# Optimization experiments

Measured on AMD Instinct MI355X. Metric: run time of the kernel, lower is better.

## Reference

```python
import jax, jax.numpy as jnp
import numpy as np

T, A, B_IMG, Z, READ_N, WRITE_N, ENC, DEC, BATCH = 16, 64, 64, 128, 8, 8, 512, 512, 512
EPS = 1e-8


def setup_inputs() -> dict:
    key = jax.random.key(0)
    ks = jax.random.split(key, 16)
    s = 0.05
    n = lambda k, shape: jax.random.normal(k, shape, jnp.float32) * s
    return {
        "x": jax.random.uniform(ks[0], (BATCH, B_IMG * A), jnp.float32),
        "eps": jax.random.normal(ks[1], (T, BATCH, Z), jnp.float32),
        "enc_Wih": n(ks[2], (4 * ENC, 2 * READ_N * READ_N + DEC)),
        "enc_Whh": n(ks[3], (4 * ENC, ENC)),
        "enc_b": jnp.zeros((4 * ENC,), jnp.float32),
        "mu_W": n(ks[4], (Z, ENC)),
        "mu_b": jnp.zeros((Z,), jnp.float32),
        "sig_W": n(ks[5], (Z, ENC)),
        "sig_b": jnp.zeros((Z,), jnp.float32),
        "dec_Wih": n(ks[6], (4 * DEC, Z)),
        "dec_Whh": n(ks[7], (4 * DEC, DEC)),
        "dec_b": jnp.zeros((4 * DEC,), jnp.float32),
        "write_W": n(ks[8], (WRITE_N * WRITE_N, DEC)),
        "write_b": jnp.zeros((WRITE_N * WRITE_N,), jnp.float32),
        "attn_W": n(ks[9], (5, DEC)),
        "attn_b": jnp.zeros((5,), jnp.float32),
    }


def _lstm(x, h, c, Wih, Whh, b):
    g = x @ Wih.T + h @ Whh.T + b  # [bs, 4H]
    i, f, gg, o = jnp.split(g, 4, axis=1)
    c2 = jax.nn.sigmoid(f) * c + jax.nn.sigmoid(i) * jnp.tanh(gg)
    return jax.nn.sigmoid(o) * jnp.tanh(c2), c2


def _filterbank(gx, gy, sigma2, delta, N):
    # gx, gy, sigma2, delta: [bs, 1]
    grid = jnp.arange(N, dtype=jnp.float32)[None, :]  # [1, N]
    mu_x = gx + (grid - 0.5 * N - 0.5) * delta  # [bs, N]
    mu_y = gy + (grid - 0.5 * N - 0.5) * delta
    a = jnp.arange(A, dtype=jnp.float32)
    b = jnp.arange(B_IMG, dtype=jnp.float32)
    s2 = sigma2[:, :, None]  # [bs,1,1]
    Fx = jnp.exp(-((a[None, None, :] - mu_x[:, :, None]) ** 2) / (2 * s2))  # [bs,N,A]
    Fx = Fx / (Fx.sum(2, keepdims=True) + EPS)
    Fy = jnp.exp(-((b[None, None, :] - mu_y[:, :, None]) ** 2) / (2 * s2))  # [bs,N,B]
    Fy = Fy / (Fy.sum(2, keepdims=True) + EPS)
    return Fx, Fy


def _attn_window(h_dec, N, attn_W, attn_b):
    p = h_dec @ attn_W.T + attn_b  # [bs,5]
    gx_, gy_, log_s2, log_d, log_g = jnp.split(p, 5, axis=1)
    gx = (A + 1) * 0.5 * (gx_ + 1)
    gy = (B_IMG + 1) * 0.5 * (gy_ + 1)
    delta = (max(A, B_IMG) - 1) * jnp.exp(log_d) / (N - 1)
    Fx, Fy = _filterbank(gx, gy, jnp.exp(log_s2), delta, N)
    return Fx, Fy, jnp.exp(log_g)  # gamma: [bs,1]


def reference(x, eps, enc_Wih, enc_Whh, enc_b, mu_W, mu_b, sig_W, sig_b,
              dec_Wih, dec_Whh, dec_b, write_W, write_b, attn_W, attn_b):
    bs = x.shape[0]
    img = x.reshape(bs, B_IMG, A)

    def step(carry, e):
        h_enc, c_enc, h_dec, c_dec, canvas = carry
        x_hat = x - jax.nn.sigmoid(canvas)
        # --- read with attention ---
        Fx, Fy, gamma = _attn_window(h_dec, READ_N, attn_W, attn_b)
        def glimpse(im):  # Fy @ im @ Fx^T -> [bs, N, N]
            g = jnp.einsum('bnh,bhw,bmw->bnm', Fy, im, Fx)
            return g.reshape(bs, READ_N * READ_N) * gamma
        r = jnp.concatenate([glimpse(img), glimpse(x_hat.reshape(bs, B_IMG, A))], axis=1)
        # --- encoder LSTM ---
        h_enc, c_enc = _lstm(jnp.concatenate([r, h_dec], 1), h_enc, c_enc, enc_Wih, enc_Whh, enc_b)
        # --- latent sample ---
        mu = h_enc @ mu_W.T + mu_b
        log_sigma = h_enc @ sig_W.T + sig_b
        z = mu + e * jnp.exp(log_sigma)
        # --- decoder LSTM ---
        h_dec, c_dec = _lstm(z, h_dec, c_dec, dec_Wih, dec_Whh, dec_b)
        # --- write with attention ---
        w = (h_dec @ write_W.T + write_b).reshape(bs, WRITE_N, WRITE_N)
        Fx2, Fy2, gamma2 = _attn_window(h_dec, WRITE_N, attn_W, attn_b)
        wr = jnp.einsum('bnh,bnm,bma->bha', Fy2, w, Fx2).reshape(bs, B_IMG * A) / gamma2
        canvas = canvas + wr
        return (h_enc, c_enc, h_dec, c_dec, canvas), canvas

    z32 = jnp.zeros((bs, ENC), jnp.float32)
    init = (z32, z32, jnp.zeros((bs, DEC), jnp.float32), jnp.zeros((bs, DEC), jnp.float32),
            jnp.zeros((bs, B_IMG * A), jnp.float32))
    _, cs = jax.lax.scan(step, init, eps)
    return cs  # [T, bs, B*A]
```

## Files before the change

kernel.cpp:

```cpp
#include <hip/hip_runtime.h>

#define LDF 68
#define EPSF 1e-8f
#define MFMA(A,B,C) __builtin_amdgcn_mfma_f32_16x16x32_bf16((A),(B),(C),0,0,0)

typedef __attribute__((ext_vector_type(8))) short bf16x8;
typedef __attribute__((ext_vector_type(4))) float f32x4;

__device__ __forceinline__ float sigf(float x){ return 1.0f/(1.0f + __expf(-x)); }

__device__ __forceinline__ unsigned short f2bf(float f){
  unsigned u = __float_as_uint(f);
  u += 0x7FFFu + ((u >> 16) & 1u);
  return (unsigned short)(u >> 16);
}
__device__ __forceinline__ float bf2f(unsigned short s){
  return __uint_as_float((unsigned)s << 16);
}

__device__ __forceinline__ size_t pk(int b, int col, int KB){
  return ((((size_t)((b>>4)*KB + (col>>5)))*64) + (size_t)((b&15) + (((col>>3)&3)<<4)))*8 + (col&7);
}

__device__ __forceinline__ void gload_lds16(const void* g, void* l){
  __builtin_amdgcn_global_load_lds(
      (const __attribute__((address_space(1))) void*)g,
      (__attribute__((address_space(3))) void*)l, 16, 0, 0);
}

__global__ void pack_w_mfma(const float* __restrict__ Wih, const float* __restrict__ Whh,
                            int K_ih, int K_tot,
                            unsigned short* __restrict__ dhi, unsigned short* __restrict__ dlo,
                            int total8){
  int idx = blockIdx.x*256 + threadIdx.x;
  if (idx >= total8) return;
  int lane = idx & 63;
  int rest = idx >> 6;
  int KB = K_tot >> 5;
  int kb = rest % KB;
  int fm = rest / KB;
  int rr = fm*16 + (lane & 15);
  int orow = (rr & 3)*512 + (rr >> 2);
  int k0 = kb*32 + (lane >> 4)*8;
  union { unsigned short s[8]; uint4 u; } vh, vl;
  #pragma unroll
  for (int i = 0; i < 8; i++){
    int k = k0 + i;
    float f = (k < K_ih) ? Wih[(size_t)orow*K_ih + k]
                         : Whh[(size_t)orow*512 + (k - K_ih)];
    unsigned short hi = f2bf(f);
    vh.s[i] = hi;
    vl.s[i] = f2bf(f - bf2f(hi));
  }
  *(uint4*)(dhi + (size_t)idx*8) = vh.u;
  *(uint4*)(dlo + (size_t)idx*8) = vl.u;
}

__global__ void init_misc(const float* __restrict__ enc_b, const float* __restrict__ dec_b,
                          const float* __restrict__ writeW,
                          const float* __restrict__ muW, const float* __restrict__ sigW,
                          float* __restrict__ bE, float* __restrict__ bD,
                          float* __restrict__ WwT,
                          unsigned short* __restrict__ Wzh, unsigned short* __restrict__ Wzl){
  int idx = blockIdx.x*256 + threadIdx.x;
  if (idx < 2048){
    bE[idx] = enc_b[(idx & 3)*512 + (idx >> 2)];
    return;
  }
  idx -= 2048;
  if (idx < 2048){
    bD[idx] = dec_b[(idx & 3)*512 + (idx >> 2)];
    return;
  }
  idx -= 2048;
  if (idx < 32768){
    int k = idx >> 6, n = idx & 63;
    WwT[idx] = writeW[n*512 + k];
    return;
  }
  idx -= 32768;
  if (idx < 16384){
    int lane = idx & 63, rest = idx >> 6;
    int kb = rest & 15, fmf = rest >> 4;
    int row = fmf*16 + (lane & 15);
    const float* src = (row < 128) ? (muW + (size_t)row*512) : (sigW + (size_t)(row-128)*512);
    int k0 = kb*32 + (lane >> 4)*8;
    union { unsigned short s[8]; uint4 u; } vh, vl;
    #pragma unroll
    for (int i = 0; i < 8; i++){
      float f = src[k0 + i];
      unsigned short hi = f2bf(f);
      vh.s[i] = hi;
      vl.s[i] = f2bf(f - bf2f(hi));
    }
    *(uint4*)(Wzh + (size_t)idx*8) = vh.u;
    *(uint4*)(Wzl + (size_t)idx*8) = vl.u;
  }
}

__global__ void zero_f(float* p, int n){
  int idx = blockIdx.x*256 + threadIdx.x;
  if (idx < n) p[idx] = 0.f;
}

template<int KB>
__global__ __launch_bounds__(512) void mfma_gemm_lstm(
    const bf16x8* __restrict__ Wh, const bf16x8* __restrict__ Wl,
    const unsigned short* __restrict__ act, int actPlane,
    const float4* __restrict__ bias4, const float* __restrict__ c_in,
    float* __restrict__ h_f32, float* __restrict__ c_out,
    unsigned short* __restrict__ out0, int KB0, int off0, int plane0,
    unsigned short* __restrict__ out1, int KB1, int off1, int plane1)
{
  __shared__ __align__(16) unsigned char lds[3][8192];
  const int tid = threadIdx.x, lane = tid & 63, w = tid >> 6;
  const int mt = blockIdx.x & 31, nt = blockIdx.x >> 5;
  const int fm = w & 3, fn0 = (w >> 2) << 1;

  const bf16x8* whp = Wh + ((size_t)(mt*4+fm)*KB)*64 + lane;
  const bf16x8* wlp = Wl + ((size_t)(mt*4+fm)*KB)*64 + lane;
  const char* ast = (const char*)act + (size_t)(w & 1)*((size_t)actPlane*2)
                  + ((size_t)(nt*4 + (w >> 1))*KB)*1024 + (size_t)lane*16;

  const int j0 = (mt*4+fm)*4 + (lane >> 4);
  float4 bb = bias4[j0];
  f32x4 acc0 = {bb.x, bb.y, bb.z, bb.w};
  f32x4 acc1 = acc0;

  gload_lds16(ast, (char*)&lds[0][w*1024]);
  bf16x8 whA = whp[0], wlA = wlp[0];
  __builtin_amdgcn_sched_barrier(0);
  asm volatile("" ::: "memory");
  gload_lds16(ast + 1024, (char*)&lds[1][w*1024]);
  bf16x8 whB = whp[64], wlB = wlp[64];
  __builtin_amdgcn_sched_barrier(0);
  asm volatile("" ::: "memory");

  const size_t rdoff = (size_t)fn0*2048 + (size_t)lane*16;

  #pragma unroll
  for (int kb = 0; kb < KB; kb++){
    if (kb + 1 < KB) asm volatile("s_waitcnt vmcnt(3)" ::: "memory");
    else             asm volatile("s_waitcnt vmcnt(0)" ::: "memory");
    __builtin_amdgcn_s_barrier();
    asm volatile("" ::: "memory");
    __builtin_amdgcn_sched_barrier(0);
    bf16x8 whC = whA, wlC = wlA;
    if (kb + 2 < KB){
      gload_lds16(ast + (size_t)(kb+2)*1024, (char*)&lds[(kb+2)%3][w*1024]);
      whC = whp[(kb+2)*64]; wlC = wlp[(kb+2)*64];
    }
    const unsigned char* rb = &lds[kb%3][0] + rdoff;
    bf16x8 a0h = *(const bf16x8*)(rb);
    bf16x8 a0l = *(const bf16x8*)(rb + 1024);
    bf16x8 a1h = *(const bf16x8*)(rb + 2048);
    bf16x8 a1l = *(const bf16x8*)(rb + 3072);
    acc0 = MFMA(whA, a0h, acc0);
    acc1 = MFMA(whA, a1h, acc1);
    acc0 = MFMA(wlA, a0h, acc0);
    acc1 = MFMA(wlA, a1h, acc1);
    acc0 = MFMA(whA, a0l, acc0);
    acc1 = MFMA(whA, a1l, acc1);
    whA = whB; wlA = wlB; whB = whC; wlB = wlC;
  }

  const int bb0 = nt*64 + fn0*16 + (lane & 15);
  #pragma unroll
  for (int n = 0; n < 2; n++){
    f32x4 g = n ? acc1 : acc0;
    int b = bb0 + n*16;
    float ig = sigf(g[0]);
    float fg = sigf(g[1]);
    float gg = tanhf(g[2]);
    float og = sigf(g[3]);
    float c2 = fg * c_in[(size_t)b*512 + j0] + ig * gg;
    float h  = og * tanhf(c2);
    c_out[(size_t)b*512 + j0] = c2;
    if (h_f32) h_f32[(size_t)b*512 + j0] = h;
    unsigned short hh = f2bf(h);
    unsigned short hl = f2bf(h - bf2f(hh));
    size_t o0 = pk(b, off0 + j0, KB0);
    out0[o0] = hh; out0[o0 + plane0] = hl;
    if (out1){
      size_t o1 = pk(b, off1 + j0, KB1);
      out1[o1] = hh; out1[o1 + plane1] = hl;
    }
  }
}

__global__ __launch_bounds__(512) void zgemm8(
    const unsigned short* __restrict__ Wzh, const unsigned short* __restrict__ Wzl,
    const unsigned short* __restrict__ az, int planeZ,
    const float* __restrict__ mu_b, const float* __restrict__ sig_b,
    const float* __restrict__ eps_t,
    unsigned short* __restrict__ actD, int planeD)
{
  __shared__ float zred[8*64*8];
  const int tid = threadIdx.x, lane = tid & 63, w = tid >> 6;
  const int fmb = blockIdx.x & 7, cg = blockIdx.x >> 3;
  const char* azh = (const char*)az + (size_t)cg*16384 + (size_t)lane*16;
  const char* azl = (const char*)(az + planeZ) + (size_t)cg*16384 + (size_t)lane*16;
  const int kb0 = w*2;

  bf16x8 a0h = *(const bf16x8*)(azh + (size_t)kb0*1024);
  bf16x8 a0l = *(const bf16x8*)(azl + (size_t)kb0*1024);
  bf16x8 a1h = *(const bf16x8*)(azh + (size_t)(kb0+1)*1024);
  bf16x8 a1l = *(const bf16x8*)(azl + (size_t)(kb0+1)*1024);

  const bf16x8* wmh = (const bf16x8*)Wzh + (size_t)(fmb    *16)*64 + lane;
  const bf16x8* wml = (const bf16x8*)Wzl + (size_t)(fmb    *16)*64 + lane;
  const bf16x8* wsh = (const bf16x8*)Wzh + (size_t)((fmb+8)*16)*64 + lane;
  const bf16x8* wsl = (const bf16x8*)Wzl + (size_t)((fmb+8)*16)*64 + lane;
  bf16x8 m0h = wmh[kb0*64],     m0l = wml[kb0*64];
  bf16x8 s0h = wsh[kb0*64],     s0l = wsl[kb0*64];
  bf16x8 m1h = wmh[(kb0+1)*64], m1l = wml[(kb0+1)*64];
  bf16x8 s1h = wsh[(kb0+1)*64], s1l = wsl[(kb0+1)*64];

  f32x4 am = {0.f,0.f,0.f,0.f}, as = {0.f,0.f,0.f,0.f};
  am = MFMA(m0h,a0h,am); am = MFMA(m0l,a0h,am); am = MFMA(m0h,a0l,am);
  as = MFMA(s0h,a0h,as); as = MFMA(s0l,a0h,as); as = MFMA(s0h,a0l,as);
  am = MFMA(m1h,a1h,am); am = MFMA(m1l,a1h,am); am = MFMA(m1h,a1l,am);
  as = MFMA(s1h,a1h,as); as = MFMA(s1l,a1h,as); as = MFMA(s1h,a1l,as);

  *(f32x4*)&zred[(size_t)(w*64+lane)*8]     = am;
  *(f32x4*)&zred[(size_t)(w*64+lane)*8 + 4] = as;
  __syncthreads();

  if (w == 0){
    const int r0 = fmb*16 + (lane >> 4)*4;
    float4 bm = *(const float4*)&mu_b[r0];
    float4 bs = *(const float4*)&sig_b[r0];
    f32x4 AM = {bm.x,bm.y,bm.z,bm.w};
    f32x4 AS = {bs.x,bs.y,bs.z,bs.w};
    #pragma unroll
    for (int v = 0; v < 8; v++){
      AM += *(f32x4*)&zred[(size_t)(v*64+lane)*8];
      AS += *(f32x4*)&zred[(size_t)(v*64+lane)*8 + 4];
    }
    const int b = cg*16 + (lane & 15);
    float4 ev = *(const float4*)&eps_t[(size_t)b*128 + r0];
    float e[4] = {ev.x, ev.y, ev.z, ev.w};
    union { unsigned short s[4]; uint2 u; } zh, zl;
    #pragma unroll
    for (int i = 0; i < 4; i++){
      float z = AM[i] + e[i]*__expf(AS[i]);
      unsigned short hi = f2bf(z);
      zh.s[i] = hi;
      zl.s[i] = f2bf(z - bf2f(hi));
    }
    size_t o = pk(b, r0, 20);
    *(uint2*)(actD + o) = zh.u;
    *(uint2*)(actD + planeD + o) = zl.u;
  }
}

__device__ void attn_window(const float* __restrict__ h,
                            const float* __restrict__ attn_W,
                            const float* __restrict__ attn_b,
                            float* Fx, float* Fy, float* pl)
{
  int tid = threadIdx.x;
  int lane = tid & 63, wid = tid >> 6;
  for (int q = wid; q < 5; q += 4){
    float s = 0.f;
    for (int k = lane; k < 512; k += 64) s += h[k]*attn_W[q*512 + k];
    for (int m = 32; m; m >>= 1) s += __shfl_xor(s, m);
    if (lane == 0) pl[q] = s + attn_b[q];
  }
  __syncthreads();
  float gx    = 32.5f*(pl[0] + 1.f);
  float gy    = 32.5f*(pl[1] + 1.f);
  float s2    = __expf(pl[2]);
  float delta = 9.f*__expf(pl[3]);
  float inv2  = 1.f/(2.f*s2);
  int n = tid >> 5, a = tid & 31;
  float mux = gx + ((float)n - 4.5f)*delta;
  float muy = gy + ((float)n - 4.5f)*delta;
  float dx0 = (float)a      - mux, dx1 = (float)(a+32) - mux;
  float dy0 = (float)a      - muy, dy1 = (float)(a+32) - muy;
  float e0 = __expf(-dx0*dx0*inv2), e1 = __expf(-dx1*dx1*inv2);
  float f0 = __expf(-dy0*dy0*inv2), f1 = __expf(-dy1*dy1*inv2);
  float sx = e0 + e1, sy = f0 + f1;
  for (int m = 16; m; m >>= 1){ sx += __shfl_xor(sx, m); sy += __shfl_xor(sy, m); }
  float rx = 1.f/(sx + EPSF), ry = 1.f/(sy + EPSF);
  Fx[n*LDF + a]      = e0*rx;  Fx[n*LDF + a + 32] = e1*rx;
  Fy[n*LDF + a]      = f0*ry;  Fy[n*LDF + a + 32] = f1*ry;
  __syncthreads();
}

__global__ __launch_bounds__(256) void wg_kernel(
    const float* __restrict__ h_dec,
    const float* __restrict__ WwT, const float* __restrict__ write_b,
    const float* __restrict__ attn_W, const float* __restrict__ attn_b,
    const float* __restrict__ canvas_prev, float* __restrict__ canvas_out,
    const float* __restrict__ x,
    unsigned short* __restrict__ rout, int planeE)
{
  __shared__ float hs[512];
  __shared__ float Fx[8*LDF], Fy[8*LDF], pl[8];
  __shared__ float cs[64*LDF];
  __shared__ float img_s[64*LDF];
  __shared__ float P[2][8*LDF];
  __shared__ float ps[4][64], w_s[64];
  __shared__ float tmp[64*8];
  const int b = blockIdx.x, tid = threadIdx.x;

  for (int i = tid; i < 128; i += 256)
    ((float4*)hs)[i] = ((const float4*)(h_dec + (size_t)b*512))[i];
  if (rout){
    const float4* x4 = (const float4*)(x + (size_t)b*4096);
    for (int i = tid; i < 1024; i += 256){
      int row = i >> 4, cb = (i & 15)*4;
      *(float4*)&img_s[row*LDF + cb] = x4[i];
    }
  }
  __syncthreads();
  attn_window(hs, attn_W, attn_b, Fx, Fy, pl);
  float gamma = __expf(pl[4]);

  if (canvas_out){
    {
      int j = tid & 63, part = tid >> 6;
      float s = 0.f;
      int kb = part*128;
      for (int k = 0; k < 128; k++) s += hs[kb + k] * WwT[(kb + k)*64 + j];
      ps[part][j] = s;
    }
    __syncthreads();
    if (tid < 64)
      w_s[tid] = write_b[tid] + ps[0][tid] + ps[1][tid] + ps[2][tid] + ps[3][tid];
    __syncthreads();
    float inv_g = __expf(-pl[4]);
    #pragma unroll
    for (int e = 0; e < 2; e++){
      int gi = e*256 + tid;
      int m = gi & 7, hh = gi >> 3;
      float s = 0.f;
      #pragma unroll
      for (int nn = 0; nn < 8; nn++) s += Fy[nn*LDF + hh] * w_s[nn*8 + m];
      tmp[hh*8 + m] = s;
    }
    __syncthreads();
    for (int e = 0; e < 16; e++){
      int idx = e*256 + tid;
      int hh = idx >> 6, a = idx & 63;
      float s = 0.f;
      #pragma unroll
      for (int m = 0; m < 8; m++) s += tmp[hh*8 + m] * Fx[m*LDF + a];
      float prev = canvas_prev ? canvas_prev[(size_t)b*4096 + idx] : 0.f;
      float cv = prev + s*inv_g;
      canvas_out[(size_t)b*4096 + idx] = cv;
      cs[hh*LDF + a] = cv;
    }
  } else {
    for (int e = 0; e < 16; e++){
      int idx = e*256 + tid;
      cs[(idx >> 6)*LDF + (idx & 63)] = 0.f;
    }
  }
  if (!rout) return;
  __syncthreads();
  for (int e = 0; e < 16; e++){
    int idx = e*256 + tid;
    int hh = idx >> 6, a = idx & 63;
    cs[hh*LDF + a] = sigf(cs[hh*LDF + a]);
  }
  __syncthreads();
  #pragma unroll
  for (int e = 0; e < 4; e++){
    int gi = e*256 + tid;
    int d = gi >> 9, rem = gi & 511;
    int m = rem & 7, hh = rem >> 3;
    const float* S = d ? cs : img_s;
    float s = 0.f;
    #pragma unroll
    for (int w4 = 0; w4 < 64; w4 += 4){
      float4 iv = *(const float4*)&S[hh*LDF + w4];
      float4 fv = *(const float4*)&Fx[m*LDF + w4];
      s += iv.x*fv.x + iv.y*fv.y + iv.z*fv.z + iv.w*fv.w;
    }
    P[d][m*LDF + hh] = s;
  }
  __syncthreads();
  if (tid < 128){
    int d = tid >> 6, l = tid & 63;
    int n = l >> 3, m = l & 7;
    float s = 0.f;
    #pragma unroll
    for (int h4 = 0; h4 < 64; h4 += 4){
      float4 fv = *(const float4*)&Fy[n*LDF + h4];
      float4 pv = *(const float4*)&P[d][m*LDF + h4];
      s += fv.x*pv.x + fv.y*pv.y + fv.z*pv.z + fv.w*pv.w;
    }
    tmp[d*64 + l] = s;
  }
  __syncthreads();
  if (tid < 64){
    float g1 = tmp[tid]*gamma;
    float g2 = (tmp[tid] - tmp[64 + tid])*gamma;
    unsigned short h1 = f2bf(g1), l1 = f2bf(g1 - bf2f(h1));
    unsigned short h2 = f2bf(g2), l2 = f2bf(g2 - bf2f(h2));
    size_t o1 = pk(b, tid, 36);
    size_t o2 = pk(b, 64 + tid, 36);
    rout[o1] = h1; rout[o1 + planeE] = l1;
    rout[o2] = h2; rout[o2 + planeE] = l2;
  }
}

extern "C" void kernel_launch(void* const* d_in, const int* in_sizes, int n_in,
                              void* d_out, int out_size, void* d_ws, size_t ws_size,
                              hipStream_t stream)
{
  (void)in_sizes; (void)n_in; (void)out_size; (void)ws_size;
  const float* x       = (const float*)d_in[0];
  const float* eps     = (const float*)d_in[1];
  const float* encWih  = (const float*)d_in[2];
  const float* encWhh  = (const float*)d_in[3];
  const float* enc_b   = (const float*)d_in[4];
  const float* muW     = (const float*)d_in[5];
  const float* mu_b    = (const float*)d_in[6];
  const float* sigW    = (const float*)d_in[7];
  const float* sig_b   = (const float*)d_in[8];
  const float* decWih  = (const float*)d_in[9];
  const float* decWhh  = (const float*)d_in[10];
  const float* dec_b   = (const float*)d_in[11];
  const float* writeW  = (const float*)d_in[12];
  const float* write_b = (const float*)d_in[13];
  const float* attnW   = (const float*)d_in[14];
  const float* attn_b  = (const float*)d_in[15];
  float* out = (float*)d_out;

  char* p = (char*)d_ws;
  auto alloc = [&](size_t bytes){ char* r = p; p += (bytes + 255) & ~(size_t)255; return r; };

  const int KE = 1152, KD = 640;
  const int PE = 512*KE, PD = 512*KD, PZ = 512*512;
  const int T8E = 128*36*64, T8D = 128*20*64;

  unsigned short* WpEh = (unsigned short*)alloc((size_t)T8E*16);
  unsigned short* WpEl = (unsigned short*)alloc((size_t)T8E*16);
  unsigned short* WpDh = (unsigned short*)alloc((size_t)T8D*16);
  unsigned short* WpDl = (unsigned short*)alloc((size_t)T8D*16);
  unsigned short* Wzh  = (unsigned short*)alloc(16384*16);
  unsigned short* Wzl  = (unsigned short*)alloc(16384*16);
  float* bE  = (float*)alloc(2048*4);
  float* bD  = (float*)alloc(2048*4);
  float* WwT = (float*)alloc(512*64*4);
  char* z0 = p;
  unsigned short* actE0 = (unsigned short*)alloc((size_t)2*PE*2);
  unsigned short* actD0 = (unsigned short*)alloc((size_t)2*PD*2);
  float* hDf = (float*)alloc(512*512*4);
  float* cE0 = (float*)alloc(512*512*4);
  float* cD0 = (float*)alloc(512*512*4);
  size_t zbytes = (size_t)(p - z0);
  unsigned short* actE1 = (unsigned short*)alloc((size_t)2*PE*2);
  unsigned short* actD1 = (unsigned short*)alloc((size_t)2*PD*2);
  unsigned short* AZ    = (unsigned short*)alloc((size_t)2*PZ*2);
  float* cE1 = (float*)alloc(512*512*4);
  float* cD1 = (float*)alloc(512*512*4);

  unsigned short* actE[2] = { actE0, actE1 };
  unsigned short* actD[2] = { actD0, actD1 };
  float* cEf[2] = { cE0, cE1 };
  float* cDf[2] = { cD0, cD1 };

  int tot;
  tot = T8E;   pack_w_mfma<<<(tot+255)/256,256,0,stream>>>(encWih, encWhh, 640, KE, WpEh, WpEl, tot);
  tot = T8D;   pack_w_mfma<<<(tot+255)/256,256,0,stream>>>(decWih, decWhh, 128, KD, WpDh, WpDl, tot);
  tot = 2048+2048+32768+16384;
  init_misc<<<(tot+255)/256,256,0,stream>>>(enc_b, dec_b, writeW, muW, sigW,
                                            bE, bD, WwT, Wzh, Wzl);
  tot = (int)(zbytes/4); zero_f<<<(tot+255)/256,256,0,stream>>>((float*)z0, tot);

  wg_kernel<<<512,256,0,stream>>>(hDf, WwT, write_b, attnW, attn_b,
                                  nullptr, nullptr, x, actE[0], PE);

  for (int t = 0; t < 16; t++){
    int cur = t & 1, nxt = cur ^ 1;

    mfma_gemm_lstm<36><<<256,512,0,stream>>>(
        (const bf16x8*)WpEh, (const bf16x8*)WpEl, actE[cur], PE,
        (const float4*)bE, cEf[cur], nullptr, cEf[nxt],
        AZ, 16, 0, PZ,
        actE[nxt], 36, 640, PE);

    zgemm8<<<256,512,0,stream>>>(
        Wzh, Wzl, AZ, PZ, mu_b, sig_b,
        eps + (size_t)t*65536, actD[cur], PD);

    mfma_gemm_lstm<20><<<256,512,0,stream>>>(
        (const bf16x8*)WpDh, (const bf16x8*)WpDl, actD[cur], PD,
        (const float4*)bD, cDf[cur], hDf, cDf[nxt],
        actE[nxt], 36, 128, PE,
        actD[nxt], 20, 128, PD);

    wg_kernel<<<512,256,0,stream>>>(hDf, WwT, write_b, attnW, attn_b,
                                    t ? (out + (size_t)(t-1)*2097152) : nullptr,
                                    out + (size_t)t*2097152, x,
                                    (t < 15) ? actE[nxt] : nullptr, PE);
  }
}
```

Before: 881.6 us.

## Process two k-blocks per pipeline stage in LSTM GEMM and use fast tanh

Restructures the LSTM MFMA GEMM pipeline so each stage loads and consumes two k-blocks, halving the barrier and wait overhead per iteration, and doubles the LDS stage buffers accordingly. Adds a launch bound hint for occupancy and replaces tanhf with an exp-based fast approximation in the gate epilogue. The change risks register pressure and slightly different numerics near tanh saturation, and it assumes KB is even.

Measured after the change: 889.7 us. No clear change (+0.9%).

```diff
diff --git a/kernel.cpp b/kernel.cpp
--- a/kernel.cpp
+++ b/kernel.cpp
@@ -8,6 +8,7 @@
 typedef __attribute__((ext_vector_type(4))) float f32x4;
 
 __device__ __forceinline__ float sigf(float x){ return 1.0f/(1.0f + __expf(-x)); }
+__device__ __forceinline__ float tanhfast(float x){ return 1.f - 2.f/(1.f + __expf(2.f*x)); }
 
 __device__ __forceinline__ unsigned short f2bf(float f){
   unsigned u = __float_as_uint(f);
@@ -104,7 +105,7 @@
 }
 
 template<int KB>
-__global__ __launch_bounds__(512) void mfma_gemm_lstm(
+__global__ __launch_bounds__(512, 4) void mfma_gemm_lstm(
     const bf16x8* __restrict__ Wh, const bf16x8* __restrict__ Wl,
     const unsigned short* __restrict__ act, int actPlane,
     const float4* __restrict__ bias4, const float* __restrict__ c_in,
@@ -112,7 +113,8 @@
     unsigned short* __restrict__ out0, int KB0, int off0, int plane0,
     unsigned short* __restrict__ out1, int KB1, int off1, int plane1)
 {
-  __shared__ __align__(16) unsigned char lds[3][8192];
+  constexpr int NI = KB/2;
+  __shared__ __align__(16) unsigned char lds[3][16384];
   const int tid = threadIdx.x, lane = tid & 63, w = tid >> 6;
   const int mt = blockIdx.x & 31, nt = blockIdx.x >> 5;
   const int fm = w & 3, fn0 = (w >> 2) << 1;
@@ -127,41 +129,60 @@
   f32x4 acc0 = {bb.x, bb.y, bb.z, bb.w};
   f32x4 acc1 = acc0;
 
-  gload_lds16(ast, (char*)&lds[0][w*1024]);
-  bf16x8 whA = whp[0], wlA = wlp[0];
+  bf16x8 wh[2][2], wl[2][2];
+
+  wh[0][0] = whp[0];  wh[0][1] = whp[64];
+  wl[0][0] = wlp[0];  wl[0][1] = wlp[64];
   __builtin_amdgcn_sched_barrier(0);
-  asm volatile("" ::: "memory");
-  gload_lds16(ast + 1024, (char*)&lds[1][w*1024]);
-  bf16x8 whB = whp[64], wlB = wlp[64];
+  {
+    char* d0 = (char*)&lds[0][w*2048];
+    gload_lds16(ast,        d0);
+    gload_lds16(ast + 1024, d0 + 1024);
+  }
   __builtin_amdgcn_sched_barrier(0);
-  asm volatile("" ::: "memory");
-
-  const size_t rdoff = (size_t)fn0*2048 + (size_t)lane*16;
+  {
+    char* d1 = (char*)&lds[1][w*2048];
+    gload_lds16(ast + 2048, d1);
+    gload_lds16(ast + 3072, d1 + 1024);
+  }
+  __builtin_amdgcn_sched_barrier(0);
+
+  const size_t rdbase = (size_t)fn0*4096 + (size_t)lane*16;
 
   #pragma unroll
-  for (int kb = 0; kb < KB; kb++){
-    if (kb + 1 < KB) asm volatile("s_waitcnt vmcnt(3)" ::: "memory");
-    else             asm volatile("s_waitcnt vmcnt(0)" ::: "memory");
+  for (int i = 0; i < NI; i++){
+    if (i + 1 < NI) asm volatile("s_waitcnt vmcnt(2)" ::: "memory");
+    else            asm volatile("s_waitcnt vmcnt(0)" ::: "memory");
     __builtin_amdgcn_s_barrier();
-    asm volatile("" ::: "memory");
     __builtin_amdgcn_sched_barrier(0);
-    bf16x8 whC = whA, wlC = wlA;
-    if (kb + 2 < KB){
-      gload_lds16(ast + (size_t)(kb+2)*1024, (char*)&lds[(kb+2)%3][w*1024]);
-      whC = whp[(kb+2)*64]; wlC = wlp[(kb+2)*64];
-    }
-    const unsigned char* rb = &lds[kb%3][0] + rdoff;
-    bf16x8 a0h = *(const bf16x8*)(rb);
-    bf16x8 a0l = *(const bf16x8*)(rb + 1024);
-    bf16x8 a1h = *(const bf16x8*)(rb + 2048);
-    bf16x8 a1l = *(const bf16x8*)(rb + 3072);
-    acc0 = MFMA(whA, a0h, acc0);
-    acc1 = MFMA(whA, a1h, acc1);
-    acc0 = MFMA(wlA, a0h, acc0);
-    acc1 = MFMA(wlA, a1h, acc1);
-    acc0 = MFMA(whA, a0l, acc0);
-    acc1 = MFMA(whA, a1l, acc1);
-    whA = whB; wlA = wlB; whB = whC; wlB = wlC;
+    if (i + 1 < NI){
+      wh[(i+1)&1][0] = whp[(2*i+2)*64];
+      wh[(i+1)&1][1] = whp[(2*i+3)*64];
+      wl[(i+1)&1][0] = wlp[(2*i+2)*64];
+      wl[(i+1)&1][1] = wlp[(2*i+3)*64];
+    }
+    __builtin_amdgcn_sched_barrier(0);
+    if (i + 2 < NI){
+      char* dst = (char*)&lds[(i+2)%3][w*2048];
+      gload_lds16(ast + (size_t)(2*i+4)*1024, dst);
+      gload_lds16(ast + (size_t)(2*i+5)*1024, dst + 1024);
+    }
+    __builtin_amdgcn_sched_barrier(0);
+    const unsigned char* rb = &lds[i%3][0] + rdbase;
+    #pragma unroll
+    for (int kbi = 0; kbi < 2; kbi++){
+      bf16x8 a0h = *(const bf16x8*)(rb +        kbi*1024);
+      bf16x8 a0l = *(const bf16x8*)(rb + 2048 + kbi*1024);
+      bf16x8 a1h = *(const bf16x8*)(rb + 4096 + kbi*1024);
+      bf16x8 a1l = *(const bf16x8*)(rb + 6144 + kbi*1024);
+      bf16x8 WH = wh[i&1][kbi], WL = wl[i&1][kbi];
+      acc0 = MFMA(WH, a0h, acc0);
+      acc1 = MFMA(WH, a1h, acc1);
+      acc0 = MFMA(WL, a0h, acc0);
+      acc1 = MFMA(WL, a1h, acc1);
+      acc0 = MFMA(WH, a0l, acc0);
+      acc1 = MFMA(WH, a1l, acc1);
+    }
   }
 
   const int bb0 = nt*64 + fn0*16 + (lane & 15);
@@ -171,10 +192,10 @@
     int b = bb0 + n*16;
     float ig = sigf(g[0]);
     float fg = sigf(g[1]);
-    float gg = tanhf(g[2]);
+    float gg = tanhfast(g[2]);
     float og = sigf(g[3]);
     float c2 = fg * c_in[(size_t)b*512 + j0] + ig * gg;
-    float h  = og * tanhf(c2);
+    float h  = og * tanhfast(c2);
     c_out[(size_t)b*512 + j0] = c2;
     if (h_f32) h_f32[(size_t)b*512 + j0] = h;
     unsigned short hh = f2bf(h);
```

## Fuse decoder LSTM GEMM with write/glimpse kernel via per-batch-tile grid barrier

Applied to the files above, without the earlier changes.

Merges the decoder LSTM GEMM and the attention write/read kernel into one launch. Blocks that share a batch tile sync through a global atomic counter, then each block handles the write and glimpse stage for two batch rows, reading h_dec with cache-bypassing loads. This removes one kernel launch and its gap per timestep and lets the write work start per tile instead of after the whole GEMM. It also swaps tanhf for an exp-based fast tanh. The spin barrier assumes all 32 blocks of a tile are co-resident, so the code risks deadlock and a little precision loss.

Measured after the change: 1.008 ms. 14.3% more time.

```diff
diff --git a/kernel.cpp b/kernel.cpp
--- a/kernel.cpp
+++ b/kernel.cpp
@@ -8,6 +8,7 @@
 typedef __attribute__((ext_vector_type(4))) float f32x4;
 
 __device__ __forceinline__ float sigf(float x){ return 1.0f/(1.0f + __expf(-x)); }
+__device__ __forceinline__ float tanhfast(float x){ return 1.f - 2.f/(1.f + __expf(2.f*x)); }
 
 __device__ __forceinline__ unsigned short f2bf(float f){
   unsigned u = __float_as_uint(f);
@@ -26,6 +27,15 @@
   __builtin_amdgcn_global_load_lds(
       (const __attribute__((address_space(1))) void*)g,
       (__attribute__((address_space(3))) void*)l, 16, 0, 0);
+}
+
+__device__ __forceinline__ uint4 ld_x4_sc(const void* p){
+  uint4 r;
+  asm volatile("global_load_dwordx4 %0, %1, off sc0 sc1" : "=v"(r) : "v"(p));
+  return r;
+}
+__device__ __forceinline__ void st_dword_sc(void* p, float v){
+  asm volatile("global_store_dword %0, %1, off sc0 sc1" :: "v"(p), "v"(v) : "memory");
 }
 
 __global__ void pack_w_mfma(const float* __restrict__ Wih, const float* __restrict__ Whh,
@@ -104,15 +114,15 @@
 }
 
 template<int KB>
-__global__ __launch_bounds__(512) void mfma_gemm_lstm(
+__device__ __forceinline__ void gemm_body(
+    unsigned char (&lds)[3][8192],
     const bf16x8* __restrict__ Wh, const bf16x8* __restrict__ Wl,
     const unsigned short* __restrict__ act, int actPlane,
     const float4* __restrict__ bias4, const float* __restrict__ c_in,
-    float* __restrict__ h_f32, float* __restrict__ c_out,
+    float* __restrict__ h_sc, float* __restrict__ c_out,
     unsigned short* __restrict__ out0, int KB0, int off0, int plane0,
     unsigned short* __restrict__ out1, int KB1, int off1, int plane1)
 {
-  __shared__ __align__(16) unsigned char lds[3][8192];
   const int tid = threadIdx.x, lane = tid & 63, w = tid >> 6;
   const int mt = blockIdx.x & 31, nt = blockIdx.x >> 5;
   const int fm = w & 3, fn0 = (w >> 2) << 1;
@@ -171,12 +181,12 @@
     int b = bb0 + n*16;
     float ig = sigf(g[0]);
     float fg = sigf(g[1]);
-    float gg = tanhf(g[2]);
+    float gg = tanhfast(g[2]);
     float og = sigf(g[3]);
     float c2 = fg * c_in[(size_t)b*512 + j0] + ig * gg;
-    float h  = og * tanhf(c2);
+    float h  = og * tanhfast(c2);
     c_out[(size_t)b*512 + j0] = c2;
-    if (h_f32) h_f32[(size_t)b*512 + j0] = h;
+    if (h_sc) st_dword_sc(h_sc + (size_t)b*512 + j0, h);
     unsigned short hh = f2bf(h);
     unsigned short hl = f2bf(h - bf2f(hh));
     size_t o0 = pk(b, off0 + j0, KB0);
@@ -186,6 +196,20 @@
       out1[o1] = hh; out1[o1 + plane1] = hl;
     }
   }
+}
+
+template<int KB>
+__global__ __launch_bounds__(512) void mfma_gemm_lstm(
+    const bf16x8* __restrict__ Wh, const bf16x8* __restrict__ Wl,
+    const unsigned short* __restrict__ act, int actPlane,
+    const float4* __restrict__ bias4, const float* __restrict__ c_in,
+    float* __restrict__ h_sc, float* __restrict__ c_out,
+    unsigned short* __restrict__ out0, int KB0, int off0, int plane0,
+    unsigned short* __restrict__ out1, int KB1, int off1, int plane1)
+{
+  __shared__ __align__(16) unsigned char lds[3][8192];
+  gemm_body<KB>(lds, Wh, Wl, act, actPlane, bias4, c_in, h_sc, c_out,
+                out0, KB0, off0, plane0, out1, KB1, off1, plane1);
 }
 
 __global__ __launch_bounds__(512) void zgemm8(
@@ -254,26 +278,34 @@
   }
 }
 
-__device__ void attn_window(const float* __restrict__ h,
-                            const float* __restrict__ attn_W,
-                            const float* __restrict__ attn_b,
-                            float* Fx, float* Fy, float* pl)
-{
-  int tid = threadIdx.x;
-  int lane = tid & 63, wid = tid >> 6;
+struct WgS {
+  float hs[512];
+  float Fx[8*LDF], Fy[8*LDF], pl[8];
+  float cs[64*LDF];
+  float img_s[64*LDF];
+  float P[2][8*LDF];
+  float ps[4][64], w_s[64];
+  float tmp[64*8];
+};
+
+__device__ void attn_window2(WgS& S, int t,
+                             const float* __restrict__ attn_W,
+                             const float* __restrict__ attn_b)
+{
+  int lane = t & 63, wid = t >> 6;
   for (int q = wid; q < 5; q += 4){
     float s = 0.f;
-    for (int k = lane; k < 512; k += 64) s += h[k]*attn_W[q*512 + k];
+    for (int k = lane; k < 512; k += 64) s += S.hs[k]*attn_W[q*512 + k];
     for (int m = 32; m; m >>= 1) s += __shfl_xor(s, m);
-    if (lane == 0) pl[q] = s + attn_b[q];
+    if (lane == 0) S.pl[q] = s + attn_b[q];
   }
   __syncthreads();
-  float gx    = 32.5f*(pl[0] + 1.f);
-  float gy    = 32.5f*(pl[1] + 1.f);
-  float s2    = __expf(pl[2]);
-  float delta = 9.f*__expf(pl[3]);
+  float gx    = 32.5f*(S.pl[0] + 1.f);
+  float gy    = 32.5f*(S.pl[1] + 1.f);
+  float s2    = __expf(S.pl[2]);
+  float delta = 9.f*__expf(S.pl[3]);
   float inv2  = 1.f/(2.f*s2);
-  int n = tid >> 5, a = tid & 31;
+  int n = t >> 5, a = t & 31;
   float mux = gx + ((float)n - 4.5f)*delta;
   float muy = gy + ((float)n - 4.5f)*delta;
   float dx0 = (float)a      - mux, dx1 = (float)(a+32) - mux;
@@ -283,12 +315,12 @@
   float sx = e0 + e1, sy = f0 + f1;
   for (int m = 16; m; m >>= 1){ sx += __shfl_xor(sx, m); sy += __shfl_xor(sy, m); }
   float rx = 1.f/(sx + EPSF), ry = 1.f/(sy + EPSF);
-  Fx[n*LDF + a]      = e0*rx;  Fx[n*LDF + a + 32] = e1*rx;
-  Fy[n*LDF + a]      = f0*ry;  Fy[n*LDF + a + 32] = f1*ry;
+  S.Fx[n*LDF + a]      = e0*rx;  S.Fx[n*LDF + a + 32] = e1*rx;
+  S.Fy[n*LDF + a]      = f0*ry;  S.Fy[n*LDF + a + 32] = f1*ry;
   __syncthreads();
 }
 
-__global__ __launch_bounds__(256) void wg_kernel(
+__device__ void wg_phase(WgS& S, int t, int b,
     const float* __restrict__ h_dec,
     const float* __restrict__ WwT, const float* __restrict__ write_b,
     const float* __restrict__ attn_W, const float* __restrict__ attn_b,
@@ -296,115 +328,166 @@
     const float* __restrict__ x,
     unsigned short* __restrict__ rout, int planeE)
 {
-  __shared__ float hs[512];
-  __shared__ float Fx[8*LDF], Fy[8*LDF], pl[8];
-  __shared__ float cs[64*LDF];
-  __shared__ float img_s[64*LDF];
-  __shared__ float P[2][8*LDF];
-  __shared__ float ps[4][64], w_s[64];
-  __shared__ float tmp[64*8];
-  const int b = blockIdx.x, tid = threadIdx.x;
-
-  for (int i = tid; i < 128; i += 256)
-    ((float4*)hs)[i] = ((const float4*)(h_dec + (size_t)b*512))[i];
+  uint4 rh = {0,0,0,0};
+  if (t < 128)
+    rh = ld_x4_sc((const char*)(h_dec + (size_t)b*512) + (size_t)t*16);
   if (rout){
     const float4* x4 = (const float4*)(x + (size_t)b*4096);
-    for (int i = tid; i < 1024; i += 256){
+    for (int i = t; i < 1024; i += 256){
       int row = i >> 4, cb = (i & 15)*4;
-      *(float4*)&img_s[row*LDF + cb] = x4[i];
-    }
-  }
+      *(float4*)&S.img_s[row*LDF + cb] = x4[i];
+    }
+  }
+  asm volatile("s_waitcnt vmcnt(0)" ::: "memory");
+  __builtin_amdgcn_sched_barrier(0);
+  if (t < 128) *(uint4*)&S.hs[t*4] = rh;
   __syncthreads();
-  attn_window(hs, attn_W, attn_b, Fx, Fy, pl);
-  float gamma = __expf(pl[4]);
+  attn_window2(S, t, attn_W, attn_b);
+  float gamma = __expf(S.pl[4]);
 
   if (canvas_out){
     {
-      int j = tid & 63, part = tid >> 6;
+      int j = t & 63, part = t >> 6;
       float s = 0.f;
       int kb = part*128;
-      for (int k = 0; k < 128; k++) s += hs[kb + k] * WwT[(kb + k)*64 + j];
-      ps[part][j] = s;
-    }
-    __syncthreads();
-    if (tid < 64)
-      w_s[tid] = write_b[tid] + ps[0][tid] + ps[1][tid] + ps[2][tid] + ps[3][tid];
-    __syncthreads();
-    float inv_g = __expf(-pl[4]);
+      for (int k = 0; k < 128; k++) s += S.hs[kb + k] * WwT[(kb + k)*64 + j];
+      S.ps[part][j] = s;
+    }
+    __syncthreads();
+    if (t < 64)
+      S.w_s[t] = write_b[t] + S.ps[0][t] + S.ps[1][t] + S.ps[2][t] + S.ps[3][t];
+    __syncthreads();
+    float inv_g = __expf(-S.pl[4]);
     #pragma unroll
     for (int e = 0; e < 2; e++){
-      int gi = e*256 + tid;
+      int gi = e*256 + t;
       int m = gi & 7, hh = gi >> 3;
       float s = 0.f;
       #pragma unroll
-      for (int nn = 0; nn < 8; nn++) s += Fy[nn*LDF + hh] * w_s[nn*8 + m];
-      tmp[hh*8 + m] = s;
+      for (int nn = 0; nn < 8; nn++) s += S.Fy[nn*LDF + hh] * S.w_s[nn*8 + m];
+      S.tmp[hh*8 + m] = s;
     }
     __syncthreads();
     for (int e = 0; e < 16; e++){
-      int idx = e*256 + tid;
+      int idx = e*256 + t;
       int hh = idx >> 6, a = idx & 63;
       float s = 0.f;
       #pragma unroll
-      for (int m = 0; m < 8; m++) s += tmp[hh*8 + m] * Fx[m*LDF + a];
+      for (int m = 0; m < 8; m++) s += S.tmp[hh*8 + m] * S.Fx[m*LDF + a];
       float prev = canvas_prev ? canvas_prev[(size_t)b*4096 + idx] : 0.f;
       float cv = prev + s*inv_g;
       canvas_out[(size_t)b*4096 + idx] = cv;
-      cs[hh*LDF + a] = cv;
+      S.cs[hh*LDF + a] = cv;
     }
   } else {
     for (int e = 0; e < 16; e++){
-      int idx = e*256 + tid;
-      cs[(idx >> 6)*LDF + (idx & 63)] = 0.f;
-    }
-  }
-  if (!rout) return;
+      int idx = e*256 + t;
+      S.cs[(idx >> 6)*LDF + (idx & 63)] = 0.f;
+    }
+  }
+
+  if (rout){
+    __syncthreads();
+    for (int e = 0; e < 16; e++){
+      int idx = e*256 + t;
+      int hh = idx >> 6, a = idx & 63;
+      S.cs[hh*LDF + a] = sigf(S.cs[hh*LDF + a]);
+    }
+    __syncthreads();
+    #pragma unroll
+    for (int e = 0; e < 4; e++){
+      int gi = e*256 + t;
+      int d = gi >> 9, rem = gi & 511;
+      int m = rem & 7, hh = rem >> 3;
+      const float* Ssrc = d ? S.cs : S.img_s;
+      float s = 0.f;
+      #pragma unroll
+      for (int w4 = 0; w4 < 64; w4 += 4){
+        float4 iv = *(const float4*)&Ssrc[hh*LDF + w4];
+        float4 fv = *(const float4*)&S.Fx[m*LDF + w4];
+        s += iv.x*fv.x + iv.y*fv.y + iv.z*fv.z + iv.w*fv.w;
+      }
+      S.P[d][m*LDF + hh] = s;
+    }
+    __syncthreads();
+    if (t < 128){
+      int d = t >> 6, l = t & 63;
+      int n = l >> 3, m = l & 7;
+      float s = 0.f;
+      #pragma unroll
+      for (int h4 = 0; h4 < 64; h4 += 4){
+        float4 fv = *(const float4*)&S.Fy[n*LDF + h4];
+        float4 pv = *(const float4*)&S.P[d][m*LDF + h4];
+        s += fv.x*pv.x + fv.y*pv.y + fv.z*pv.z + fv.w*pv.w;
+      }
+      S.tmp[d*64 + l] = s;
+    }
+    __syncthreads();
+    if (t < 64){
+      float g1 = S.tmp[t]*gamma;
+      float g2 = (S.tmp[t] - S.tmp[64 + t])*gamma;
+      unsigned short h1 = f2bf(g1), l1 = f2bf(g1 - bf2f(h1));
+      unsigned short h2 = f2bf(g2), l2 = f2bf(g2 - bf2f(h2));
+      size_t o1 = pk(b, t, 36);
+      size_t o2 = pk(b, 64 + t, 36);
+      rout[o1] = h1; rout[o1 + planeE] = l1;
+      rout[o2] = h2; rout[o2 + planeE] = l2;
+    }
+  }
+}
+
+__global__ __launch_bounds__(256) void wg0_kernel(
+    const float* __restrict__ h_dec, const float* __restrict__ WwT,
+    const float* __restrict__ write_b,
+    const float* __restrict__ attn_W, const float* __restrict__ attn_b,
+    const float* __restrict__ x, unsigned short* __restrict__ rout, int planeE)
+{
+  __shared__ WgS S;
+  wg_phase(S, threadIdx.x, blockIdx.x, h_dec, WwT, write_b, attn_W, attn_b,
+           nullptr, nullptr, x, rout, planeE);
+}
+
+union DecSM {
+  unsigned char glds[3][8192];
+  WgS wg[2];
+};
+
+__global__ __launch_bounds__(512) void dec_wg(
+    const bf16x8* __restrict__ Wh, const bf16x8* __restrict__ Wl,
+    const unsigned short* __restrict__ act, int actPlane,
+    const float4* __restrict__ bias4, const float* __restrict__ c_in,
+    float* __restrict__ hD_sc, float* __restrict__ c_out,
+    unsigned short* __restrict__ out0, int KB0, int off0, int plane0,
+    unsigned short* __restrict__ out1, int KB1, int off1, int plane1,
+    const float* __restrict__ WwT, const float* __restrict__ write_b,
+    const float* __restrict__ attnW, const float* __restrict__ attn_b,
+    const float* __restrict__ canvas_prev, float* __restrict__ canvas_out,
+    const float* __restrict__ x,
+    unsigned short* __restrict__ rout, int planeE,
+    unsigned int* __restrict__ bar)
+{
+  __shared__ __align__(16) DecSM sm;
+
+  gemm_body<20>(sm.glds, Wh, Wl, act, actPlane, bias4, c_in, hD_sc, c_out,
+                out0, KB0, off0, plane0, out1, KB1, off1, plane1);
+
+  asm volatile("s_waitcnt vmcnt(0) lgkmcnt(0)" ::: "memory");
   __syncthreads();
-  for (int e = 0; e < 16; e++){
-    int idx = e*256 + tid;
-    int hh = idx >> 6, a = idx & 63;
-    cs[hh*LDF + a] = sigf(cs[hh*LDF + a]);
+  const int nt = blockIdx.x >> 5;
+  if (threadIdx.x == 0){
+    unsigned int* cell = bar + nt*16;
+    __hip_atomic_fetch_add(cell, 1u, __ATOMIC_RELAXED, __HIP_MEMORY_SCOPE_AGENT);
+    while (__hip_atomic_load(cell, __ATOMIC_RELAXED, __HIP_MEMORY_SCOPE_AGENT) < 32u)
+      __builtin_amdgcn_s_sleep(8);
   }
   __syncthreads();
-  #pragma unroll
-  for (int e = 0; e < 4; e++){
-    int gi = e*256 + tid;
-    int d = gi >> 9, rem = gi & 511;
-    int m = rem & 7, hh = rem >> 3;
-    const float* S = d ? cs : img_s;
-    float s = 0.f;
-    #pragma unroll
-    for (int w4 = 0; w4 < 64; w4 += 4){
-      float4 iv = *(const float4*)&S[hh*LDF + w4];
-      float4 fv = *(const float4*)&Fx[m*LDF + w4];
-      s += iv.x*fv.x + iv.y*fv.y + iv.z*fv.z + iv.w*fv.w;
-    }
-    P[d][m*LDF + hh] = s;
-  }
-  __syncthreads();
-  if (tid < 128){
-    int d = tid >> 6, l = tid & 63;
-    int n = l >> 3, m = l & 7;
-    float s = 0.f;
-    #pragma unroll
-    for (int h4 = 0; h4 < 64; h4 += 4){
-      float4 fv = *(const float4*)&Fy[n*LDF + h4];
-      float4 pv = *(const float4*)&P[d][m*LDF + h4];
-      s += fv.x*pv.x + fv.y*pv.y + fv.z*pv.z + fv.w*pv.w;
-    }
-    tmp[d*64 + l] = s;
-  }
-  __syncthreads();
-  if (tid < 64){
-    float g1 = tmp[tid]*gamma;
-    float g2 = (tmp[tid] - tmp[64 + tid])*gamma;
-    unsigned short h1 = f2bf(g1), l1 = f2bf(g1 - bf2f(h1));
-    unsigned short h2 = f2bf(g2), l2 = f2bf(g2 - bf2f(h2));
-    size_t o1 = pk(b, tid, 36);
-    size_t o2 = pk(b, 64 + tid, 36);
-    rout[o1] = h1; rout[o1 + planeE] = l1;
-    rout[o2] = h2; rout[o2 + planeE] = l2;
-  }
+
+  const int tid = threadIdx.x;
+  const int half = tid >> 8, t256 = tid & 255;
+  const int mt = blockIdx.x & 31;
+  const int b2 = nt*64 + mt*2 + half;
+  wg_phase(sm.wg[half], t256, b2, hD_sc, WwT, write_b, attnW, attn_b,
+           canvas_prev, canvas_out, x, rout, planeE);
 }
 
 extern "C" void kernel_launch(void* const* d_in, const int* in_sizes, int n_in,
@@ -447,6 +530,7 @@
   float* bD  = (float*)alloc(2048*4);
   float* WwT = (float*)alloc(512*64*4);
   char* z0 = p;
+  unsigned int* bar = (unsigned int*)alloc(16*8*16*4);
   unsigned short* actE0 = (unsigned short*)alloc((size_t)2*PE*2);
   unsigned short* actD0 = (unsigned short*)alloc((size_t)2*PD*2);
   float* hDf = (float*)alloc(512*512*4);
@@ -472,8 +556,7 @@
                                             bE, bD, WwT, Wzh, Wzl);
   tot = (int)(zbytes/4); zero_f<<<(tot+255)/256,256,0,stream>>>((float*)z0, tot);
 
-  wg_kernel<<<512,256,0,stream>>>(hDf, WwT, write_b, attnW, attn_b,
-                                  nullptr, nullptr, x, actE[0], PE);
+  wg0_kernel<<<512,256,0,stream>>>(hDf, WwT, write_b, attnW, attn_b, x, actE[0], PE);
 
   for (int t = 0; t < 16; t++){
     int cur = t & 1, nxt = cur ^ 1;
@@ -488,15 +571,15 @@
         Wzh, Wzl, AZ, PZ, mu_b, sig_b,
         eps + (size_t)t*65536, actD[cur], PD);
 
-    mfma_gemm_lstm<20><<<256,512,0,stream>>>(
+    dec_wg<<<256,512,0,stream>>>(
         (const bf16x8*)WpDh, (const bf16x8*)WpDl, actD[cur], PD,
         (const float4*)bD, cDf[cur], hDf, cDf[nxt],
         actE[nxt], 36, 128, PE,
-        actD[nxt], 20, 128, PD);
-
-    wg_kernel<<<512,256,0,stream>>>(hDf, WwT, write_b, attnW, attn_b,
-                                    t ? (out + (size_t)(t-1)*2097152) : nullptr,
-                                    out + (size_t)t*2097152, x,
-                                    (t < 15) ? actE[nxt] : nullptr, PE);
-  }
-}
+        actD[nxt], 20, 128, PD,
+        WwT, write_b, attnW, attn_b,
+        t ? (out + (size_t)(t-1)*2097152) : nullptr,
+        out + (size_t)t*2097152, x,
+        (t < 15) ? actE[nxt] : nullptr, PE,
+        bar + t*8*16);
+  }
+}
```
